# Optimization experiments

Measured on AMD Instinct MI355X. Metric: run time of the kernel, lower is better.

Reference implementation:

```python
import jax, jax.numpy as jnp
import numpy as np

N = 20000    # nodes
F = 64       # channels (num_features)
Z = 10       # species
DEG = 16
E = N * DEG  # edges
RD = 8       # radial_dim
EPS = 0.25   # epsilon (avg-degree normalization)
SQRT3 = 3.0 ** 0.5


def setup_inputs() -> dict:
    key = jax.random.key(0)
    ks = jax.random.split(key, 22)
    g = lambda i, shape, s=1.0: jax.random.normal(ks[i], shape, jnp.float32) * s
    return dict(
        vectors=g(0, (E, 3)),
        node_s=g(1, (N, F)),
        node_v=g(2, (N, F, 3)),
        radial_embed=jax.random.uniform(ks[3], (E, RD), jnp.float32),
        senders=jax.random.randint(ks[4], (E,), 0, N),
        receivers=jax.random.randint(ks[5], (E,), 0, N),
        species_counts=jnp.full((Z,), N // Z, dtype=jnp.int32),
        Wup0=g(6, (F, F)), Wup1=g(7, (F, F)),
        R1=g(8, (RD, 64)), R2=g(9, (64, 64)), R3=g(10, (64, 64)), R4=g(11, (64, 4 * F)),
        Wd0=g(12, (F, F)), Wd1=g(13, (F, F)),
        Ws0=g(14, (Z, F, F)), Ws1=g(15, (Z, F, F)),
        Wsc=g(16, (Z, 9, F)), Proj=g(17, (9, 9), 1.0 / 3.0),
        Wl0=g(18, (F, F)), Wl1=g(19, (F, F)),
        Wr=g(20, (F, 1)),
    )


def _forward(vectors, node_s, node_v, radial_embed, senders, receivers,
             species_counts, Wup0, Wup1, R1, R2, R3, R4, Wd0, Wd1,
             Ws0, Ws1, Wsc, Proj, Wl0, Wl1, Wr):
    inv = 1.0 / np.sqrt(F)
    # species index per node (counts -> contiguous blocks), like jnp.repeat in SymmetricContraction
    sidx = jnp.repeat(jnp.arange(Z), species_counts, total_repeat_length=N)

    # spherical harmonics l=0 (constant 1, folded into weights) and l=1
    r = jnp.linalg.norm(vectors, axis=-1, keepdims=True)
    Y1 = SQRT3 * vectors / r                              # (E,3)

    # species-indexed skip connection on input feats
    skip_s = jnp.einsum('nf,nfg->ng', node_s, Ws0[sidx]) * inv
    skip_v = jnp.einsum('nfi,nfg->ngi', node_v, Ws1[sidx]) * inv

    # linear_up (per-irrep channel mixing)
    hs = (node_s @ Wup0) * inv                            # (N,F)
    hv = jnp.einsum('nfi,fg->ngi', node_v, Wup1) * inv    # (N,F,3)

    # radial MLP -> per-edge, per-path, per-channel TP weights (weight_numel = 4*F)
    a = jax.nn.silu(radial_embed @ R1)
    a = jax.nn.silu(a @ R2)
    a = jax.nn.silu(a @ R3)
    w = (a @ R4).reshape(E, 4, F)

    # channelwise tensor product: gather senders, 4 CG paths, scatter to receivers
    es = hs[senders]                                      # (E,F)
    ev = hv[senders]                                      # (E,F,3)
    m_s = w[:, 0] * es + w[:, 1] * (jnp.einsum('efi,ei->ef', ev, Y1) / SQRT3)
    m_v = w[:, 2][..., None] * ev + w[:, 3][..., None] * (es[..., None] * Y1[:, None, :]) / SQRT3
    hs = jax.ops.segment_sum(m_s, receivers, num_segments=N) * EPS
    hv = jax.ops.segment_sum(m_v, receivers, num_segments=N) * EPS

    # linear_down
    hs = (hs @ Wd0) * inv
    hv = jnp.einsum('nfi,fg->ngi', hv, Wd1) * inv

    # symmetric contraction (correlation 1..3), species-keyed weights through fixed projection
    wsc = jnp.einsum('zpu,pb->zbu', Wsc, Proj)[sidx]      # (N,9,F)
    vv = jnp.sum(hv * hv, -1)                             # (N,F)
    bs = jnp.stack([hs, hs * hs, vv, hs ** 3, hs * vv], axis=1)                    # (N,5,F)
    bv = jnp.stack([hv, hs[..., None] * hv, (hs * hs)[..., None] * hv,
                    vv[..., None] * hv], axis=1)                                   # (N,4,F,3)
    cs = jnp.einsum('nbf,nbf->nf', bs, wsc[:, :5])
    cv = jnp.einsum('nbfi,nbf->nfi', bv, wsc[:, 5:])

    # linear_sc
    cs = (cs @ Wl0) * inv
    cv = jnp.einsum('nfi,fg->ngi', cv, Wl1) * inv

    # add skip
    h_s = cs + skip_s
    h_v = cv + skip_v

    # readout (0e -> 1x0e; only scalars participate)
    out = (h_s @ Wr) * inv                                # (N,1)
    return out, h_s, h_v


def reference(vectors, node_s, node_v, radial_embed, senders, receivers,
              species_counts, Wup0, Wup1, R1, R2, R3, R4, Wd0, Wd1,
              Ws0, Ws1, Wsc, Proj, Wl0, Wl1, Wr):
    return _forward(vectors, node_s, node_v, radial_embed, senders, receivers,
                    species_counts, Wup0, Wup1, R1, R2, R3, R4, Wd0, Wd1,
                    Ws0, Ws1, Wsc, Proj, Wl0, Wl1, Wr)
```

## Files before the change

kernel.cpp:

```cpp
#include <hip/hip_runtime.h>
#include <hip/hip_bf16.h>
#include <hip/hip_fp16.h>
#include <math.h>

#define N_NODES 20000
#define FCH 64
#define ZSP 10
#define E_EDGES 320000
#define CHUNK 160000
#define RDIM 8
#define EPSC 0.25f
#define SQRT3C 1.7320508075688772f
#define INV_SQRT3C 0.57735026918962576f
#define INV_F 0.125f

#define OFF_EUP    0
#define OFF_SKS    (N_NODES*256)
#define OFF_SKV    (OFF_SKS + N_NODES*64)
#define OFF_HSMID  (OFF_SKV + N_NODES*192)
#define OFF_HVMID  (OFF_HSMID + N_NODES*64)
#define OFF_WSCP   (OFF_HVMID + N_NODES*192)
#define OFF_FRAGS  (OFF_WSCP + ZSP*576)
#define OFF_WBUF   (OFF_FRAGS + 13312)
#define OFF_CSR    (OFF_WBUF + CHUNK*128)
#define OFF_WF     (OFF_CSR + 2*CHUNK*4 + 400260)
#define CSR_CNT0   0
#define CSR_CNT1   20000
#define CSR_PTR0   40000
#define CSR_PTR1   60001
#define CSR_SEID   80002
#define CSR_AUX    400002

#define SU_WSC   5760
#define SU_PREP  (SU_WSC + 3328)
#define SU_PREP2 (SU_PREP + 26624)
#define SU_HIST  (SU_PREP2 + E_EDGES)

typedef __attribute__((ext_vector_type(8))) short bhalf8;
typedef __attribute__((ext_vector_type(4))) float f32x4;

__device__ __forceinline__ float silu_f(float x) {
    float e = __builtin_amdgcn_exp2f(x * -1.442695040888963f);
    return x * __builtin_amdgcn_rcpf(1.0f + e);
}

__device__ __forceinline__ unsigned short f2bf(float x) {
    unsigned int u = __float_as_uint(x);
    unsigned int r = u + 0x7FFFu + ((u >> 16) & 1u);
    return (unsigned short)(r >> 16);
}

__device__ __forceinline__ unsigned int pack_bf2(float lo, float hi) {
    __hip_bfloat162 b = __float22bfloat162_rn(make_float2(lo, hi));
    return *(unsigned int*)&b;
}

__device__ __forceinline__ bhalf8 mk8(unsigned a, unsigned b, unsigned c, unsigned d) {
    uint4 u; u.x = a; u.y = b; u.z = c; u.w = d;
    return *(bhalf8*)&u;
}

__device__ __forceinline__ float half_lo(unsigned v) {
    return __half2float(__ushort_as_half((unsigned short)(v & 0xFFFFu)));
}
__device__ __forceinline__ float half_hi(unsigned v) {
    return __half2float(__ushort_as_half((unsigned short)(v >> 16)));
}

__device__ __forceinline__ void split_f32(float x, short& h, short& l) {
    unsigned int u = __float_as_uint(x);
    unsigned int hb = u & 0xFFFF0000u;
    h = (short)(u >> 16);
    float r = x - __uint_as_float(hb);
    l = (short)(__float_as_uint(r) >> 16);
}

__device__ __forceinline__ int species_of(int n, const int* counts) {
    int acc = 0, s = ZSP - 1;
#pragma unroll
    for (int z = 0; z < ZSP; z++) {
        int c = counts[z];
        if (n >= acc && n < acc + c) s = z;
        acc += c;
    }
    return s;
}

__global__ __launch_bounds__(256) void k_setup(
    const float* __restrict__ Wsc, const float* __restrict__ Proj, float* __restrict__ wscp,
    const float* __restrict__ R1, const float* __restrict__ R2,
    const float* __restrict__ R3, const float* __restrict__ R4,
    unsigned short* __restrict__ frags,
    const float* __restrict__ Wup0, const float* __restrict__ Wup1,
    const float* __restrict__ Ws0, const float* __restrict__ Ws1,
    const float* __restrict__ Wd0, const float* __restrict__ Wd1,
    const float* __restrict__ Wl0, const float* __restrict__ Wl1,
    unsigned short* __restrict__ wf,
    const int* __restrict__ receivers, int* __restrict__ csr) {
    int gid = blockIdx.x * 256 + threadIdx.x;
    if (gid < SU_WSC) {
        int z = gid / 576, t = gid % 576;
        int b = t >> 6, u = t & 63;
        float acc = 0.f;
#pragma unroll
        for (int p = 0; p < 9; p++) acc += Wsc[z * 576 + p * 64 + u] * Proj[p * 9 + b];
        wscp[z * 576 + b * 64 + u] = acc;
    } else if (gid < SU_PREP) {
        int id = gid - SU_WSC;
        int lane = id & 63, fi = id >> 6;
        int quad = lane >> 4, l15 = lane & 15;
        const float* W;
        int s, t, N;
        bool r1 = false;
        if (fi < 4)       { W = R1; s = 0; t = fi; N = 64; r1 = true; }
        else if (fi < 12) { W = R2; int x = fi - 4;  s = x >> 2; t = x & 3;  N = 64; }
        else if (fi < 20) { W = R3; int x = fi - 12; s = x >> 2; t = x & 3;  N = 64; }
        else              { W = R4; int x = fi - 20; s = x >> 4; t = x & 15; N = 256; }
        unsigned int v[4];
#pragma unroll
        for (int jj = 0; jj < 4; jj++) {
            unsigned short pk2[2];
#pragma unroll
            for (int o = 0; o < 2; o++) {
                int j = jj * 2 + o;
                int k = s * 32 + quad * 8 + j, n = t * 16 + l15;
                float val = (r1 && k >= RDIM) ? 0.f : W[k * N + n];
                pk2[o] = f2bf(val);
            }
            v[jj] = (unsigned int)pk2[0] | ((unsigned int)pk2[1] << 16);
        }
        uint4 pk; pk.x = v[0]; pk.y = v[1]; pk.z = v[2]; pk.w = v[3];
        ((uint4*)frags)[id] = pk;
    } else if (gid < SU_PREP2) {
        int id = gid - SU_PREP;
        int lane = id & 63, slot = id >> 6;
        int t = slot & 3, s = (slot >> 2) & 1, part = (slot >> 3) & 1, mat = slot >> 4;
        int quad = lane >> 4, l15 = lane & 15;
        const float* W;
        if (mat == 0)       W = Wup0;
        else if (mat == 1)  W = Wup1;
        else if (mat < 12)  W = Ws0 + (mat - 2) * 4096;
        else if (mat < 22)  W = Ws1 + (mat - 12) * 4096;
        else if (mat == 22) W = Wd0;
        else if (mat == 23) W = Wd1;
        else if (mat == 24) W = Wl0;
        else                W = Wl1;
        unsigned int v[4];
#pragma unroll
        for (int jj = 0; jj < 4; jj++) {
            unsigned short pk2[2];
#pragma unroll
            for (int o = 0; o < 2; o++) {
                int j = jj * 2 + o;
                int k = s * 32 + quad * 8 + j, n = t * 16 + l15;
                float x = W[k * 64 + n];
                short h, l;
                split_f32(x, h, l);
                pk2[o] = part == 0 ? (unsigned short)h : (unsigned short)l;
            }
            v[jj] = (unsigned int)pk2[0] | ((unsigned int)pk2[1] << 16);
        }
        uint4 pk; pk.x = v[0]; pk.y = v[1]; pk.z = v[2]; pk.w = v[3];
        ((uint4*)wf)[id] = pk;
    } else if (gid < SU_HIST) {
        int e = gid - SU_PREP2;
        int base = (e < CHUNK) ? CSR_CNT0 : CSR_CNT1;
        atomicAdd(&csr[base + receivers[e]], 1);
    }
}

__global__ __launch_bounds__(256) void k_scan1(int* __restrict__ csr) {
    __shared__ int sb[256];
    int z = blockIdx.y, b = blockIdx.x, t = threadIdx.x;
    int i = b * 256 + t;
    int cb = z ? CSR_CNT1 : CSR_CNT0;
    int pb = z ? CSR_PTR1 : CSR_PTR0;
    int x = (i < N_NODES) ? csr[cb + i] : 0;
    sb[t] = x;
    __syncthreads();
#pragma unroll
    for (int off = 1; off < 256; off <<= 1) {
        int v = (t >= off) ? sb[t - off] : 0;
        __syncthreads();
        sb[t] += v;
        __syncthreads();
    }
    if (i < N_NODES) csr[pb + i] = sb[t] - x;
    if (t == 255) csr[CSR_AUX + z * 128 + b] = sb[255];
}

__global__ __launch_bounds__(128) void k_scan2(int* __restrict__ csr) {
    __shared__ int sb[128];
    int z = blockIdx.x, t = threadIdx.x;
    int pb = z ? CSR_PTR1 : CSR_PTR0;
    int x = (t < 79) ? csr[CSR_AUX + z * 128 + t] : 0;
    sb[t] = x;
    __syncthreads();
#pragma unroll
    for (int off = 1; off < 128; off <<= 1) {
        int v = (t >= off) ? sb[t - off] : 0;
        __syncthreads();
        sb[t] += v;
        __syncthreads();
    }
    csr[CSR_AUX + z * 128 + t] = sb[t] - x;
    if (t == 127) csr[pb + N_NODES] = sb[127];
}

__global__ __launch_bounds__(256) void k_scan3(int* __restrict__ csr) {
    int z = blockIdx.y, b = blockIdx.x, t = threadIdx.x;
    int i = b * 256 + t;
    if (i >= N_NODES) return;
    int cb = z ? CSR_CNT1 : CSR_CNT0;
    int pb = z ? CSR_PTR1 : CSR_PTR0;
    int v = csr[pb + i] + csr[CSR_AUX + z * 128 + b];
    csr[pb + i] = v;
    csr[cb + i] = v;
}

__global__ __launch_bounds__(256) void k_bucket(
    const float* __restrict__ vectors, const int* __restrict__ senders,
    const int* __restrict__ receivers, int* __restrict__ csr,
    float4* __restrict__ erec) {
    int e = blockIdx.x * 256 + threadIdx.x;
    if (e >= E_EDGES) return;
    int z = (e < CHUNK) ? 0 : 1;
    int base = z ? CSR_CNT1 : CSR_CNT0;
    int pos = atomicAdd(&csr[base + receivers[e]], 1);
    float v0 = vectors[e * 3 + 0], v1 = vectors[e * 3 + 1], v2 = vectors[e * 3 + 2];
    float s = SQRT3C * rsqrtf(v0 * v0 + v1 * v1 + v2 * v2);
    int idx = z * CHUNK + pos;
    csr[CSR_SEID + idx] = e;
    float4 r;
    r.x = v0 * s; r.y = v1 * s; r.z = v2 * s; r.w = __int_as_float(senders[e]);
    erec[idx] = r;
}

__global__ __launch_bounds__(256) void k_node_pre(
    const float* __restrict__ ns, const float* __restrict__ nv,
    const int* __restrict__ counts, const unsigned short* __restrict__ wf,
    float* __restrict__ ws) {
    __shared__ uint2 eup_t[16][64];
    int tid = threadIdx.x, w = tid >> 6, lane = tid & 63;
    int q = lane >> 4, l15 = lane & 15;
    int nw = blockIdx.x * 16;
    int sid = species_of(nw, counts);
    const f32x4 z4 = {0.f, 0.f, 0.f, 0.f};

    bhalf8 Ah[2], Al[2];
    if (w == 0) {
#pragma unroll
        for (int s = 0; s < 2; s++) {
            const float* rp = ns + (size_t)(nw + l15) * 64 + s * 32 + q * 8;
            float4 a = *(const float4*)rp, b = *(const float4*)(rp + 4);
            float x[8] = {a.x, a.y, a.z, a.w, b.x, b.y, b.z, b.w};
#pragma unroll
            for (int j = 0; j < 8; j++) { short h, l; split_f32(x[j], h, l); Ah[s][j] = h; Al[s][j] = l; }
        }
    } else {
        int i = w - 1;
#pragma unroll
        for (int s = 0; s < 2; s++) {
            const float* rp = nv + (size_t)(nw + l15) * 192 + i;
#pragma unroll
            for (int j = 0; j < 8; j++) {
                float x = rp[(s * 32 + q * 8 + j) * 3];
                short h, l; split_f32(x, h, l); Ah[s][j] = h; Al[s][j] = l;
            }
        }
    }

    const bhalf8* wfv = (const bhalf8*)wf;
    float* sks = ws + OFF_SKS;
    float* skv = ws + OFF_SKV;

    {
        int mat = (w == 0) ? 0 : 1;
#pragma unroll
        for (int t = 0; t < 4; t++) {
            f32x4 acc = z4;
#pragma unroll
            for (int s = 0; s < 2; s++) {
                bhalf8 bh = wfv[(size_t)(mat * 16 + 0 + s * 4 + t) * 64 + lane];
                bhalf8 bl = wfv[(size_t)(mat * 16 + 8 + s * 4 + t) * 64 + lane];
                acc = __builtin_amdgcn_mfma_f32_16x16x32_bf16(Ah[s], bh, acc, 0, 0, 0);
                acc = __builtin_amdgcn_mfma_f32_16x16x32_bf16(Al[s], bh, acc, 0, 0, 0);
                acc = __builtin_amdgcn_mfma_f32_16x16x32_bf16(Ah[s], bl, acc, 0, 0, 0);
            }
#pragma unroll
            for (int r = 0; r < 4; r++) {
                unsigned short us = __half_as_ushort(__float2half_rn(acc[r] * INV_F));
                ((unsigned short*)&eup_t[q * 4 + r][t * 16 + l15])[w] = us;
            }
        }
    }
    {
        int mat = (w == 0) ? 2 + sid : 12 + sid;
        float* dst = (w == 0) ? sks : skv;
        int stride = (w == 0) ? 64 : 192;
        int off = (w == 0) ? 0 : (w - 1) * 64;
#pragma unroll
        for (int t = 0; t < 4; t++) {
            f32x4 acc = z4;
#pragma unroll
            for (int s = 0; s < 2; s++) {
                bhalf8 bh = wfv[(size_t)(mat * 16 + 0 + s * 4 + t) * 64 + lane];
                bhalf8 bl = wfv[(size_t)(mat * 16 + 8 + s * 4 + t) * 64 + lane];
                acc = __builtin_amdgcn_mfma_f32_16x16x32_bf16(Ah[s], bh, acc, 0, 0, 0);
                acc = __builtin_amdgcn_mfma_f32_16x16x32_bf16(Al[s], bh, acc, 0, 0, 0);
                acc = __builtin_amdgcn_mfma_f32_16x16x32_bf16(Ah[s], bl, acc, 0, 0, 0);
            }
#pragma unroll
            for (int r = 0; r < 4; r++)
                dst[(size_t)(nw + q * 4 + r) * stride + off + t * 16 + l15] = acc[r] * INV_F;
        }
    }
    __syncthreads();
    uint2* eup = (uint2*)(ws + OFF_EUP);
    for (int k = tid; k < 1024; k += 256) {
        int n = k >> 6, f = k & 63;
        eup[(size_t)(nw + n) * 64 + f] = eup_t[n][f];
    }
}

template<int S>
__device__ __forceinline__ bhalf8 xfrag(const unsigned* pkA, const unsigned* pkB,
                                        int q, int l15) {
    int L0 = ((q & 1) << 5) + l15;
    int L1 = L0 + 16;
    bool hi = (q >> 1) != 0;
    unsigned a0 = (unsigned)__shfl((int)pkA[2 * S], L0, 64);
    unsigned a1 = (unsigned)__shfl((int)pkA[2 * S + 1], L0, 64);
    unsigned b0 = (unsigned)__shfl((int)pkB[2 * S], L0, 64);
    unsigned b1 = (unsigned)__shfl((int)pkB[2 * S + 1], L0, 64);
    unsigned c0 = (unsigned)__shfl((int)pkA[2 * S], L1, 64);
    unsigned c1 = (unsigned)__shfl((int)pkA[2 * S + 1], L1, 64);
    unsigned e0 = (unsigned)__shfl((int)pkB[2 * S], L1, 64);
    unsigned e1 = (unsigned)__shfl((int)pkB[2 * S + 1], L1, 64);
    return mk8(hi ? a1 : a0, hi ? b1 : b0, hi ? c1 : c0, hi ? e1 : e0);
}

__global__ __launch_bounds__(256) void k_mlp(
    const float* __restrict__ radial, const unsigned short* __restrict__ frags,
    const int* __restrict__ csr, unsigned short* __restrict__ wbuf, int e_base) {
    __shared__ unsigned short r4lds[16384];
    int tid = threadIdx.x;
    int lane = tid & 63, w = tid >> 6, quad = lane >> 4, l15 = lane & 15;

    const uint4* r4g = (const uint4*)(frags + 20 * 64 * 8);
    uint4* r4l = (uint4*)r4lds;
    for (int i = tid; i < 2048; i += 256) r4l[i] = r4g[i];
    const bhalf8* fr = (const bhalf8*)frags;
    bhalf8 r1f[4], r2f[2][4], r3f[2][4];
#pragma unroll
    for (int t = 0; t < 4; t++) r1f[t] = fr[t * 64 + lane];
#pragma unroll
    for (int s = 0; s < 2; s++)
#pragma unroll
        for (int t = 0; t < 4; t++) {
            r2f[s][t] = fr[(4 + s * 4 + t) * 64 + lane];
            r3f[s][t] = fr[(12 + s * 4 + t) * 64 + lane];
        }
    __syncthreads();

    const f32x4 z4 = {0.f, 0.f, 0.f, 0.f};
    const bhalf8* r4f = (const bhalf8*)r4lds;

    int el0 = (blockIdx.x * 4 + w) * 16;

    bhalf8 af = {0, 0, 0, 0, 0, 0, 0, 0};
    if (quad == 0) {
        int eid = csr[CSR_SEID + e_base + el0 + l15];
        const float* rp = radial + (size_t)eid * 8;
        float4 ra = *(const float4*)rp;
        float4 rb = *(const float4*)(rp + 4);
        af[0] = (short)f2bf(ra.x); af[1] = (short)f2bf(ra.y);
        af[2] = (short)f2bf(ra.z); af[3] = (short)f2bf(ra.w);
        af[4] = (short)f2bf(rb.x); af[5] = (short)f2bf(rb.y);
        af[6] = (short)f2bf(rb.z); af[7] = (short)f2bf(rb.w);
    }
    unsigned pkA[4], pkB[4];
    {
        f32x4 acc[4];
#pragma unroll
        for (int t = 0; t < 4; t++)
            acc[t] = __builtin_amdgcn_mfma_f32_16x16x32_bf16(r1f[t], af, z4, 0, 0, 0);
#pragma unroll
        for (int t = 0; t < 4; t++) {
            pkA[t] = pack_bf2(silu_f(acc[t][0]), silu_f(acc[t][1]));
            pkB[t] = pack_bf2(silu_f(acc[t][2]), silu_f(acc[t][3]));
        }
    }
#pragma unroll
    for (int layer = 0; layer < 2; layer++) {
        bhalf8 b0 = xfrag<0>(pkA, pkB, quad, l15);
        bhalf8 b1 = xfrag<1>(pkA, pkB, quad, l15);
        f32x4 acc[4];
#pragma unroll
        for (int t = 0; t < 4; t++) {
            bhalf8 w0 = layer == 0 ? r2f[0][t] : r3f[0][t];
            bhalf8 w1 = layer == 0 ? r2f[1][t] : r3f[1][t];
            acc[t] = __builtin_amdgcn_mfma_f32_16x16x32_bf16(
                w1, b1, __builtin_amdgcn_mfma_f32_16x16x32_bf16(w0, b0, z4, 0, 0, 0), 0, 0, 0);
        }
#pragma unroll
        for (int t = 0; t < 4; t++) {
            pkA[t] = pack_bf2(silu_f(acc[t][0]), silu_f(acc[t][1]));
            pkB[t] = pack_bf2(silu_f(acc[t][2]), silu_f(acc[t][3]));
        }
    }
    {
        bhalf8 a0 = xfrag<0>(pkA, pkB, quad, l15);
        bhalf8 a1 = xfrag<1>(pkA, pkB, quad, l15);
#pragma unroll
        for (int t4 = 0; t4 < 4; t4++) {
            f32x4 p0 = __builtin_amdgcn_mfma_f32_16x16x32_bf16(
                a1, r4f[(16 + t4) * 64 + lane],
                __builtin_amdgcn_mfma_f32_16x16x32_bf16(a0, r4f[t4 * 64 + lane], z4, 0, 0, 0), 0, 0, 0);
            f32x4 p1 = __builtin_amdgcn_mfma_f32_16x16x32_bf16(
                a1, r4f[(20 + t4) * 64 + lane],
                __builtin_amdgcn_mfma_f32_16x16x32_bf16(a0, r4f[(4 + t4) * 64 + lane], z4, 0, 0, 0), 0, 0, 0);
            f32x4 p2 = __builtin_amdgcn_mfma_f32_16x16x32_bf16(
                a1, r4f[(24 + t4) * 64 + lane],
                __builtin_amdgcn_mfma_f32_16x16x32_bf16(a0, r4f[(8 + t4) * 64 + lane], z4, 0, 0, 0), 0, 0, 0);
            f32x4 p3 = __builtin_amdgcn_mfma_f32_16x16x32_bf16(
                a1, r4f[(28 + t4) * 64 + lane],
                __builtin_amdgcn_mfma_f32_16x16x32_bf16(a0, r4f[(12 + t4) * 64 + lane], z4, 0, 0, 0), 0, 0, 0);
#pragma unroll
            for (int r = 0; r < 4; r++) {
                int el = el0 + quad * 4 + r;
                int f = t4 * 16 + l15;
                uint2 pk;
                pk.x = pack_bf2(p0[r], p1[r]);
                pk.y = pack_bf2(p2[r], p3[r]);
                ((uint2*)wbuf)[(size_t)el * 64 + f] = pk;
            }
        }
    }
}

__global__ __launch_bounds__(256) void k_tp_gather(
    const unsigned short* __restrict__ wbuf, const int* __restrict__ csr,
    const float4* __restrict__ erec, float* __restrict__ ws,
    int z, int accum) {
    int tid = threadIdx.x, w = tid >> 6, f = tid & 63;
    int n = blockIdx.x * 4 + w;
    const uint2* eup = (const uint2*)(ws + OFF_EUP);
    float* hs_mid = ws + OFF_HSMID;
    float* hv_mid = ws + OFF_HVMID;
    int pb = z ? CSR_PTR1 : CSR_PTR0;
    int beg = csr[pb + n], end = csr[pb + n + 1];
    int e_base = z * CHUNK;
    float ams = 0.f, am0 = 0.f, am1 = 0.f, am2 = 0.f;

    if (beg < end) {
        int last = end - 1;
        float4 rcA = erec[e_base + beg];
        uint2 wrA = ((const uint2*)wbuf)[(size_t)beg * 64 + f];
        uint2 evA = eup[(size_t)__float_as_int(rcA.w) * 64 + f];
        int j1 = (beg + 1 < end) ? beg + 1 : last;
        float4 rcB = erec[e_base + j1];
        uint2 wrB = ((const uint2*)wbuf)[(size_t)j1 * 64 + f];
        uint2 evB = eup[(size_t)__float_as_int(rcB.w) * 64 + f];

        for (int i = beg; i < end; i++) {
            int j2 = (i + 2 < end) ? i + 2 : last;
            float4 rcC = erec[e_base + j2];
            uint2 wrC = ((const uint2*)wbuf)[(size_t)j2 * 64 + f];
            uint2 evC = eup[(size_t)__float_as_int(rcC.w) * 64 + f];
            float esA = half_lo(evA.x), eA0 = half_hi(evA.x);
            float eA1 = half_lo(evA.y), eA2 = half_hi(evA.y);
            float w0 = __uint_as_float(wrA.x << 16);
            float w1 = __uint_as_float(wrA.x & 0xFFFF0000u);
            float w2 = __uint_as_float(wrA.y << 16);
            float w3 = __uint_as_float(wrA.y & 0xFFFF0000u);
            float dot = eA0 * rcA.x + eA1 * rcA.y + eA2 * rcA.z;
            ams += w0 * esA + w1 * dot * INV_SQRT3C;
            float t3 = w3 * esA * INV_SQRT3C;
            am0 += w2 * eA0 + t3 * rcA.x;
            am1 += w2 * eA1 + t3 * rcA.y;
            am2 += w2 * eA2 + t3 * rcA.z;
            rcA = rcB; wrA = wrB; evA = evB;
            rcB = rcC; wrB = wrC; evB = evC;
        }
    }
    if (!accum) {
        hs_mid[n * 64 + f] = ams;
        hv_mid[n * 192 + f] = am0;
        hv_mid[n * 192 + 64 + f] = am1;
        hv_mid[n * 192 + 128 + f] = am2;
    } else {
        hs_mid[n * 64 + f] = (hs_mid[n * 64 + f] + ams) * EPSC;
        hv_mid[n * 192 + f] = (hv_mid[n * 192 + f] + am0) * EPSC;
        hv_mid[n * 192 + 64 + f] = (hv_mid[n * 192 + 64 + f] + am1) * EPSC;
        hv_mid[n * 192 + 128 + f] = (hv_mid[n * 192 + 128 + f] + am2) * EPSC;
    }
}

__global__ __launch_bounds__(256) void k_node_post(
    const int* __restrict__ counts, const unsigned short* __restrict__ wf,
    const float* __restrict__ Wr, float* __restrict__ ws, float* __restrict__ out) {
    __shared__ float T[4][16][68];
    int tid = threadIdx.x, w = tid >> 6, lane = tid & 63;
    int q = lane >> 4, l15 = lane & 15;
    int nw = blockIdx.x * 16;
    int sid = species_of(nw, counts);
    const f32x4 z4 = {0.f, 0.f, 0.f, 0.f};
    const bhalf8* wfv = (const bhalf8*)wf;
    const float* hs_mid = ws + OFF_HSMID;
    const float* hv_mid = ws + OFF_HVMID;
    const float* sks = ws + OFF_SKS;
    const float* skv = ws + OFF_SKV;
    const float* wscp = ws + OFF_WSCP;

    {
        const float* src = (w == 0) ? hs_mid + (size_t)nw * 64
                                    : hv_mid + (size_t)nw * 192 + (w - 1) * 64;
        int rstride = (w == 0) ? 64 : 192;
        bhalf8 Ah[2], Al[2];
#pragma unroll
        for (int s = 0; s < 2; s++) {
            const float* rp = src + (size_t)l15 * rstride + s * 32 + q * 8;
            float4 a = *(const float4*)rp, b = *(const float4*)(rp + 4);
            float x[8] = {a.x, a.y, a.z, a.w, b.x, b.y, b.z, b.w};
#pragma unroll
            for (int j = 0; j < 8; j++) { short h, l; split_f32(x[j], h, l); Ah[s][j] = h; Al[s][j] = l; }
        }
        int mat = (w == 0) ? 22 : 23;
#pragma unroll
        for (int t = 0; t < 4; t++) {
            f32x4 acc = z4;
#pragma unroll
            for (int s = 0; s < 2; s++) {
                bhalf8 bh = wfv[(size_t)(mat * 16 + 0 + s * 4 + t) * 64 + lane];
                bhalf8 bl = wfv[(size_t)(mat * 16 + 8 + s * 4 + t) * 64 + lane];
                acc = __builtin_amdgcn_mfma_f32_16x16x32_bf16(Ah[s], bh, acc, 0, 0, 0);
                acc = __builtin_amdgcn_mfma_f32_16x16x32_bf16(Al[s], bh, acc, 0, 0, 0);
                acc = __builtin_amdgcn_mfma_f32_16x16x32_bf16(Ah[s], bl, acc, 0, 0, 0);
            }
#pragma unroll
            for (int r = 0; r < 4; r++)
                T[w][q * 4 + r][t * 16 + l15] = acc[r] * INV_F;
        }
    }
    __syncthreads();

    {
        int col = tid & 63, rg = tid >> 6;
        float wv[9];
#pragma unroll
        for (int b = 0; b < 9; b++) wv[b] = wscp[sid * 576 + b * 64 + col];
#pragma unroll
        for (int rr = 0; rr < 4; rr++) {
            int row = rg * 4 + rr;
            float hs = T[0][row][col];
            float h0 = T[1][row][col], h1 = T[2][row][col], h2 = T[3][row][col];
            float vv = h0 * h0 + h1 * h1 + h2 * h2;
            float cs = wv[0] * hs + wv[1] * hs * hs + wv[2] * vv
                     + wv[3] * hs * hs * hs + wv[4] * hs * vv;
            float fv = wv[5] + wv[6] * hs + wv[7] * hs * hs + wv[8] * vv;
            T[0][row][col] = cs;
            T[1][row][col] = h0 * fv;
            T[2][row][col] = h1 * fv;
            T[3][row][col] = h2 * fv;
        }
    }
    __syncthreads();

    {
        bhalf8 Ah[2], Al[2];
#pragma unroll
        for (int s = 0; s < 2; s++) {
            const float* rp = &T[w][l15][s * 32 + q * 8];
            float4 a = *(const float4*)rp, b = *(const float4*)(rp + 4);
            float x[8] = {a.x, a.y, a.z, a.w, b.x, b.y, b.z, b.w};
#pragma unroll
            for (int j = 0; j < 8; j++) { short h, l; split_f32(x[j], h, l); Ah[s][j] = h; Al[s][j] = l; }
        }
        int mat = (w == 0) ? 24 : 25;
        float* d_hs = out + N_NODES;
        float* d_hv = out + N_NODES + N_NODES * 64;
        float p[4] = {0.f, 0.f, 0.f, 0.f};
#pragma unroll
        for (int t = 0; t < 4; t++) {
            f32x4 acc = z4;
#pragma unroll
            for (int s = 0; s < 2; s++) {
                bhalf8 bh = wfv[(size_t)(mat * 16 + 0 + s * 4 + t) * 64 + lane];
                bhalf8 bl = wfv[(size_t)(mat * 16 + 8 + s * 4 + t) * 64 + lane];
                acc = __builtin_amdgcn_mfma_f32_16x16x32_bf16(Ah[s], bh, acc, 0, 0, 0);
                acc = __builtin_amdgcn_mfma_f32_16x16x32_bf16(Al[s], bh, acc, 0, 0, 0);
                acc = __builtin_amdgcn_mfma_f32_16x16x32_bf16(Ah[s], bl, acc, 0, 0, 0);
            }
            int col = t * 16 + l15;
            if (w == 0) {
                float wr = Wr[col];
#pragma unroll
                for (int r = 0; r < 4; r++) {
                    int gn = nw + q * 4 + r;
                    float v = acc[r] * INV_F + sks[(size_t)gn * 64 + col];
                    d_hs[(size_t)gn * 64 + col] = v;
                    p[r] += v * wr;
                }
            } else {
                int i = w - 1;
#pragma unroll
                for (int r = 0; r < 4; r++) {
                    int gn = nw + q * 4 + r;
                    float v = acc[r] * INV_F + skv[(size_t)gn * 192 + i * 64 + col];
                    d_hv[(size_t)gn * 192 + col * 3 + i] = v;
                }
            }
        }
        if (w == 0) {
#pragma unroll
            for (int r = 0; r < 4; r++) {
#pragma unroll
                for (int off = 1; off < 16; off <<= 1) p[r] += __shfl_xor(p[r], off, 64);
                if (l15 == 0) out[nw + q * 4 + r] = p[r] * INV_F;
            }
        }
    }
}

extern "C" void kernel_launch(void* const* d_in, const int* in_sizes, int n_in,
                              void* d_out, int out_size, void* d_ws, size_t ws_size,
                              hipStream_t stream) {
    const float* vectors   = (const float*)d_in[0];
    const float* node_s    = (const float*)d_in[1];
    const float* node_v    = (const float*)d_in[2];
    const float* radial    = (const float*)d_in[3];
    const int*   senders   = (const int*)d_in[4];
    const int*   receivers = (const int*)d_in[5];
    const int*   counts    = (const int*)d_in[6];
    const float* Wup0 = (const float*)d_in[7];
    const float* Wup1 = (const float*)d_in[8];
    const float* R1   = (const float*)d_in[9];
    const float* R2   = (const float*)d_in[10];
    const float* R3   = (const float*)d_in[11];
    const float* R4   = (const float*)d_in[12];
    const float* Wd0  = (const float*)d_in[13];
    const float* Wd1  = (const float*)d_in[14];
    const float* Ws0  = (const float*)d_in[15];
    const float* Ws1  = (const float*)d_in[16];
    const float* Wsc  = (const float*)d_in[17];
    const float* Proj = (const float*)d_in[18];
    const float* Wl0  = (const float*)d_in[19];
    const float* Wl1  = (const float*)d_in[20];
    const float* Wr   = (const float*)d_in[21];
    float* ws  = (float*)d_ws;
    float* out = (float*)d_out;
    unsigned short* frags = (unsigned short*)(ws + OFF_FRAGS);
    unsigned short* wbuf  = (unsigned short*)(ws + OFF_WBUF);
    float4* erec = (float4*)(ws + OFF_CSR);
    int* csr = (int*)(ws + OFF_CSR + 2 * CHUNK * 4);
    unsigned short* wf = (unsigned short*)(ws + OFF_WF);

    hipMemsetAsync(csr, 0, 2 * N_NODES * sizeof(int), stream);
    k_setup<<<(SU_HIST + 255) / 256, 256, 0, stream>>>(
        Wsc, Proj, ws + OFF_WSCP, R1, R2, R3, R4, frags,
        Wup0, Wup1, Ws0, Ws1, Wd0, Wd1, Wl0, Wl1, wf, receivers, csr);
    k_scan1<<<dim3(79, 2), 256, 0, stream>>>(csr);
    k_scan2<<<2, 128, 0, stream>>>(csr);
    k_scan3<<<dim3(79, 2), 256, 0, stream>>>(csr);
    k_bucket<<<E_EDGES / 256, 256, 0, stream>>>(vectors, senders, receivers, csr, erec);
    k_node_pre<<<N_NODES / 16, 256, 0, stream>>>(node_s, node_v, counts, wf, ws);
    for (int c = 0; c < 2; c++) {
        k_mlp<<<2500, 256, 0, stream>>>(radial, frags, csr, wbuf, c * CHUNK);
        k_tp_gather<<<N_NODES / 4, 256, 0, stream>>>(wbuf, csr, erec, ws, c, c);
    }
    k_node_post<<<N_NODES / 16, 256, 0, stream>>>(counts, wf, Wr, ws, out);
}
```

Baseline: 318.2 us.

## Process all edges in one pass, merge node-pre with bucketing, store TP weights as fp16

Drops the two-chunk edge split, so the MLP and gather kernels each launch once over all edges with a single CSR. This removes the extra launches and the read-modify-write accumulation into hs_mid/hv_mid, at the cost of a larger workspace. The bucketing work is folded into the node-pre kernel by giving the extra blocks edge duty. The per-edge TP weights are packed as fp16 instead of bf16, which changes precision.

New measurement: 301.5 us. -5.2%, faster.

```diff
diff --git a/kernel.cpp b/kernel.cpp
--- a/kernel.cpp
+++ b/kernel.cpp
@@ -7,7 +7,6 @@
 #define FCH 64
 #define ZSP 10
 #define E_EDGES 320000
-#define CHUNK 160000
 #define RDIM 8
 #define EPSC 0.25f
 #define SQRT3C 1.7320508075688772f
@@ -15,21 +14,19 @@
 #define INV_F 0.125f
 
 #define OFF_EUP    0
-#define OFF_SKS    (N_NODES*256)
+#define OFF_SKS    (N_NODES*128)
 #define OFF_SKV    (OFF_SKS + N_NODES*64)
 #define OFF_HSMID  (OFF_SKV + N_NODES*192)
 #define OFF_HVMID  (OFF_HSMID + N_NODES*64)
 #define OFF_WSCP   (OFF_HVMID + N_NODES*192)
 #define OFF_FRAGS  (OFF_WSCP + ZSP*576)
 #define OFF_WBUF   (OFF_FRAGS + 13312)
-#define OFF_CSR    (OFF_WBUF + CHUNK*128)
-#define OFF_WF     (OFF_CSR + 2*CHUNK*4 + 400260)
-#define CSR_CNT0   0
-#define CSR_CNT1   20000
-#define CSR_PTR0   40000
-#define CSR_PTR1   60001
-#define CSR_SEID   80002
-#define CSR_AUX    400002
+#define OFF_CSR    (OFF_WBUF + E_EDGES*128)
+#define OFF_WF     (OFF_CSR + E_EDGES*4 + 360132)
+#define CSR_CNT    0
+#define CSR_PTR    20000
+#define CSR_SEID   40001
+#define CSR_AUX    360001
 
 #define SU_WSC   5760
 #define SU_PREP  (SU_WSC + 3328)
@@ -53,6 +50,11 @@
 __device__ __forceinline__ unsigned int pack_bf2(float lo, float hi) {
     __hip_bfloat162 b = __float22bfloat162_rn(make_float2(lo, hi));
     return *(unsigned int*)&b;
+}
+
+__device__ __forceinline__ unsigned int pack_h2(float lo, float hi) {
+    __half2 h = __floats2half2_rn(lo, hi);
+    return *(unsigned int*)&h;
 }
 
 __device__ __forceinline__ bhalf8 mk8(unsigned a, unsigned b, unsigned c, unsigned d) {
@@ -164,18 +166,15 @@
         ((uint4*)wf)[id] = pk;
     } else if (gid < SU_HIST) {
         int e = gid - SU_PREP2;
-        int base = (e < CHUNK) ? CSR_CNT0 : CSR_CNT1;
-        atomicAdd(&csr[base + receivers[e]], 1);
+        atomicAdd(&csr[CSR_CNT + receivers[e]], 1);
     }
 }
 
 __global__ __launch_bounds__(256) void k_scan1(int* __restrict__ csr) {
     __shared__ int sb[256];
-    int z = blockIdx.y, b = blockIdx.x, t = threadIdx.x;
+    int b = blockIdx.x, t = threadIdx.x;
     int i = b * 256 + t;
-    int cb = z ? CSR_CNT1 : CSR_CNT0;
-    int pb = z ? CSR_PTR1 : CSR_PTR0;
-    int x = (i < N_NODES) ? csr[cb + i] : 0;
+    int x = (i < N_NODES) ? csr[CSR_CNT + i] : 0;
     sb[t] = x;
     __syncthreads();
 #pragma unroll
@@ -185,15 +184,14 @@
         sb[t] += v;
         __syncthreads();
     }
-    if (i < N_NODES) csr[pb + i] = sb[t] - x;
-    if (t == 255) csr[CSR_AUX + z * 128 + b] = sb[255];
+    if (i < N_NODES) csr[CSR_PTR + i] = sb[t] - x;
+    if (t == 255) csr[CSR_AUX + b] = sb[255];
 }
 
 __global__ __launch_bounds__(128) void k_scan2(int* __restrict__ csr) {
     __shared__ int sb[128];
-    int z = blockIdx.x, t = threadIdx.x;
-    int pb = z ? CSR_PTR1 : CSR_PTR0;
-    int x = (t < 79) ? csr[CSR_AUX + z * 128 + t] : 0;
+    int t = threadIdx.x;
+    int x = (t < 79) ? csr[CSR_AUX + t] : 0;
     sb[t] = x;
     __syncthreads();
 #pragma unroll
@@ -203,45 +201,39 @@
         sb[t] += v;
         __syncthreads();
     }
-    csr[CSR_AUX + z * 128 + t] = sb[t] - x;
-    if (t == 127) csr[pb + N_NODES] = sb[127];
+    csr[CSR_AUX + t] = sb[t] - x;
+    if (t == 127) csr[CSR_PTR + N_NODES] = sb[127];
 }
 
 __global__ __launch_bounds__(256) void k_scan3(int* __restrict__ csr) {
-    int z = blockIdx.y, b = blockIdx.x, t = threadIdx.x;
+    int b = blockIdx.x, t = threadIdx.x;
     int i = b * 256 + t;
     if (i >= N_NODES) return;
-    int cb = z ? CSR_CNT1 : CSR_CNT0;
-    int pb = z ? CSR_PTR1 : CSR_PTR0;
-    int v = csr[pb + i] + csr[CSR_AUX + z * 128 + b];
-    csr[pb + i] = v;
-    csr[cb + i] = v;
-}
-
-__global__ __launch_bounds__(256) void k_bucket(
+    int v = csr[CSR_PTR + i] + csr[CSR_AUX + b];
+    csr[CSR_PTR + i] = v;
+    csr[CSR_CNT + i] = v;
+}
+
+__global__ __launch_bounds__(256) void k_pre_bucket(
+    const float* __restrict__ ns, const float* __restrict__ nv,
+    const int* __restrict__ counts, const unsigned short* __restrict__ wf,
     const float* __restrict__ vectors, const int* __restrict__ senders,
     const int* __restrict__ receivers, int* __restrict__ csr,
-    float4* __restrict__ erec) {
-    int e = blockIdx.x * 256 + threadIdx.x;
-    if (e >= E_EDGES) return;
-    int z = (e < CHUNK) ? 0 : 1;
-    int base = z ? CSR_CNT1 : CSR_CNT0;
-    int pos = atomicAdd(&csr[base + receivers[e]], 1);
-    float v0 = vectors[e * 3 + 0], v1 = vectors[e * 3 + 1], v2 = vectors[e * 3 + 2];
-    float s = SQRT3C * rsqrtf(v0 * v0 + v1 * v1 + v2 * v2);
-    int idx = z * CHUNK + pos;
-    csr[CSR_SEID + idx] = e;
-    float4 r;
-    r.x = v0 * s; r.y = v1 * s; r.z = v2 * s; r.w = __int_as_float(senders[e]);
-    erec[idx] = r;
-}
-
-__global__ __launch_bounds__(256) void k_node_pre(
-    const float* __restrict__ ns, const float* __restrict__ nv,
-    const int* __restrict__ counts, const unsigned short* __restrict__ wf,
-    float* __restrict__ ws) {
+    float4* __restrict__ erec, float* __restrict__ ws) {
     __shared__ uint2 eup_t[16][64];
-    int tid = threadIdx.x, w = tid >> 6, lane = tid & 63;
+    int tid = threadIdx.x;
+    if (blockIdx.x >= 1250) {
+        int e = (blockIdx.x - 1250) * 256 + tid;
+        int pos = atomicAdd(&csr[CSR_CNT + receivers[e]], 1);
+        float v0 = vectors[e * 3 + 0], v1 = vectors[e * 3 + 1], v2 = vectors[e * 3 + 2];
+        float s = SQRT3C * rsqrtf(v0 * v0 + v1 * v1 + v2 * v2);
+        csr[CSR_SEID + pos] = e;
+        float4 r;
+        r.x = v0 * s; r.y = v1 * s; r.z = v2 * s; r.w = __int_as_float(senders[e]);
+        erec[pos] = r;
+        return;
+    }
+    int w = tid >> 6, lane = tid & 63;
     int q = lane >> 4, l15 = lane & 15;
     int nw = blockIdx.x * 16;
     int sid = species_of(nw, counts);
@@ -342,7 +334,7 @@
 
 __global__ __launch_bounds__(256) void k_mlp(
     const float* __restrict__ radial, const unsigned short* __restrict__ frags,
-    const int* __restrict__ csr, unsigned short* __restrict__ wbuf, int e_base) {
+    const int* __restrict__ csr, unsigned short* __restrict__ wbuf) {
     __shared__ unsigned short r4lds[16384];
     int tid = threadIdx.x;
     int lane = tid & 63, w = tid >> 6, quad = lane >> 4, l15 = lane & 15;
@@ -370,7 +362,7 @@
 
     bhalf8 af = {0, 0, 0, 0, 0, 0, 0, 0};
     if (quad == 0) {
-        int eid = csr[CSR_SEID + e_base + el0 + l15];
+        int eid = csr[CSR_SEID + el0 + l15];
         const float* rp = radial + (size_t)eid * 8;
         float4 ra = *(const float4*)rp;
         float4 rb = *(const float4*)(rp + 4);
@@ -431,8 +423,8 @@
                 int el = el0 + quad * 4 + r;
                 int f = t4 * 16 + l15;
                 uint2 pk;
-                pk.x = pack_bf2(p0[r], p1[r]);
-                pk.y = pack_bf2(p2[r], p3[r]);
+                pk.x = pack_h2(p0[r], p1[r]);
+                pk.y = pack_h2(p2[r], p3[r]);
                 ((uint2*)wbuf)[(size_t)el * 64 + f] = pk;
             }
         }
@@ -441,39 +433,34 @@
 
 __global__ __launch_bounds__(256) void k_tp_gather(
     const unsigned short* __restrict__ wbuf, const int* __restrict__ csr,
-    const float4* __restrict__ erec, float* __restrict__ ws,
-    int z, int accum) {
+    const float4* __restrict__ erec, float* __restrict__ ws) {
     int tid = threadIdx.x, w = tid >> 6, f = tid & 63;
     int n = blockIdx.x * 4 + w;
     const uint2* eup = (const uint2*)(ws + OFF_EUP);
     float* hs_mid = ws + OFF_HSMID;
     float* hv_mid = ws + OFF_HVMID;
-    int pb = z ? CSR_PTR1 : CSR_PTR0;
-    int beg = csr[pb + n], end = csr[pb + n + 1];
-    int e_base = z * CHUNK;
+    int beg = csr[CSR_PTR + n], end = csr[CSR_PTR + n + 1];
     float ams = 0.f, am0 = 0.f, am1 = 0.f, am2 = 0.f;
 
     if (beg < end) {
         int last = end - 1;
-        float4 rcA = erec[e_base + beg];
+        float4 rcA = erec[beg];
         uint2 wrA = ((const uint2*)wbuf)[(size_t)beg * 64 + f];
         uint2 evA = eup[(size_t)__float_as_int(rcA.w) * 64 + f];
         int j1 = (beg + 1 < end) ? beg + 1 : last;
-        float4 rcB = erec[e_base + j1];
+        float4 rcB = erec[j1];
         uint2 wrB = ((const uint2*)wbuf)[(size_t)j1 * 64 + f];
         uint2 evB = eup[(size_t)__float_as_int(rcB.w) * 64 + f];
 
         for (int i = beg; i < end; i++) {
             int j2 = (i + 2 < end) ? i + 2 : last;
-            float4 rcC = erec[e_base + j2];
+            float4 rcC = erec[j2];
             uint2 wrC = ((const uint2*)wbuf)[(size_t)j2 * 64 + f];
             uint2 evC = eup[(size_t)__float_as_int(rcC.w) * 64 + f];
             float esA = half_lo(evA.x), eA0 = half_hi(evA.x);
             float eA1 = half_lo(evA.y), eA2 = half_hi(evA.y);
-            float w0 = __uint_as_float(wrA.x << 16);
-            float w1 = __uint_as_float(wrA.x & 0xFFFF0000u);
-            float w2 = __uint_as_float(wrA.y << 16);
-            float w3 = __uint_as_float(wrA.y & 0xFFFF0000u);
+            float w0 = half_lo(wrA.x), w1 = half_hi(wrA.x);
+            float w2 = half_lo(wrA.y), w3 = half_hi(wrA.y);
             float dot = eA0 * rcA.x + eA1 * rcA.y + eA2 * rcA.z;
             ams += w0 * esA + w1 * dot * INV_SQRT3C;
             float t3 = w3 * esA * INV_SQRT3C;
@@ -484,17 +471,10 @@
             rcB = rcC; wrB = wrC; evB = evC;
         }
     }
-    if (!accum) {
-        hs_mid[n * 64 + f] = ams;
-        hv_mid[n * 192 + f] = am0;
-        hv_mid[n * 192 + 64 + f] = am1;
-        hv_mid[n * 192 + 128 + f] = am2;
-    } else {
-        hs_mid[n * 64 + f] = (hs_mid[n * 64 + f] + ams) * EPSC;
-        hv_mid[n * 192 + f] = (hv_mid[n * 192 + f] + am0) * EPSC;
-        hv_mid[n * 192 + 64 + f] = (hv_mid[n * 192 + 64 + f] + am1) * EPSC;
-        hv_mid[n * 192 + 128 + f] = (hv_mid[n * 192 + 128 + f] + am2) * EPSC;
-    }
+    hs_mid[n * 64 + f] = ams * EPSC;
+    hv_mid[n * 192 + f] = am0 * EPSC;
+    hv_mid[n * 192 + 64 + f] = am1 * EPSC;
+    hv_mid[n * 192 + 128 + f] = am2 * EPSC;
 }
 
 __global__ __launch_bounds__(256) void k_node_post(
@@ -653,21 +633,19 @@
     unsigned short* frags = (unsigned short*)(ws + OFF_FRAGS);
     unsigned short* wbuf  = (unsigned short*)(ws + OFF_WBUF);
     float4* erec = (float4*)(ws + OFF_CSR);
-    int* csr = (int*)(ws + OFF_CSR + 2 * CHUNK * 4);
+    int* csr = (int*)(ws + OFF_CSR + (size_t)E_EDGES * 4);
     unsigned short* wf = (unsigned short*)(ws + OFF_WF);
 
-    hipMemsetAsync(csr, 0, 2 * N_NODES * sizeof(int), stream);
+    hipMemsetAsync(csr + CSR_CNT, 0, N_NODES * sizeof(int), stream);
     k_setup<<<(SU_HIST + 255) / 256, 256, 0, stream>>>(
         Wsc, Proj, ws + OFF_WSCP, R1, R2, R3, R4, frags,
         Wup0, Wup1, Ws0, Ws1, Wd0, Wd1, Wl0, Wl1, wf, receivers, csr);
-    k_scan1<<<dim3(79, 2), 256, 0, stream>>>(csr);
-    k_scan2<<<2, 128, 0, stream>>>(csr);
-    k_scan3<<<dim3(79, 2), 256, 0, stream>>>(csr);
-    k_bucket<<<E_EDGES / 256, 256, 0, stream>>>(vectors, senders, receivers, csr, erec);
-    k_node_pre<<<N_NODES / 16, 256, 0, stream>>>(node_s, node_v, counts, wf, ws);
-    for (int c = 0; c < 2; c++) {
-        k_mlp<<<2500, 256, 0, stream>>>(radial, frags, csr, wbuf, c * CHUNK);
-        k_tp_gather<<<N_NODES / 4, 256, 0, stream>>>(wbuf, csr, erec, ws, c, c);
-    }
+    k_scan1<<<79, 256, 0, stream>>>(csr);
+    k_scan2<<<1, 128, 0, stream>>>(csr);
+    k_scan3<<<79, 256, 0, stream>>>(csr);
+    k_pre_bucket<<<2500, 256, 0, stream>>>(node_s, node_v, counts, wf,
+                                           vectors, senders, receivers, csr, erec, ws);
+    k_mlp<<<5000, 256, 0, stream>>>(radial, frags, csr, wbuf);
+    k_tp_gather<<<N_NODES / 4, 256, 0, stream>>>(wbuf, csr, erec, ws);
     k_node_post<<<N_NODES / 16, 256, 0, stream>>>(counts, wf, Wr, ws, out);
 }
```
